# Kernel optimization log

Measured on AMD Instinct MI355X. Metric: run time of the kernel, lower is better.

## Reference

```python
import jax, jax.numpy as jnp
import numpy as np

OFFSETS = (12, 20, 30, 42, 55, 67)  # pixel offsets along shadow direction


def _bilinear_shift(img, dx, dy):
    """Sample img (H,W) at (y+dy, x+dx), bilinear, zero padding.
    Equivalent to F.grid_sample with identity affine_grid + uniform shift
    (align_corners=True): normalized shift d*2/(W-1) == d pixels.
    Separable interpolation (valid because padding is zeros)."""
    H, W = img.shape
    xs = jnp.arange(W, dtype=img.dtype) + dx  # (W,) sample x-coords
    ys = jnp.arange(H, dtype=img.dtype) + dy  # (H,) sample y-coords
    x0f = jnp.floor(xs); wx = xs - x0f
    y0f = jnp.floor(ys); wy = ys - y0f
    x0 = x0f.astype(jnp.int32); x1 = x0 + 1
    y0 = y0f.astype(jnp.int32); y1 = y0 + 1

    def gx(ix):  # gather columns with zero padding
        valid = ((ix >= 0) & (ix < W)).astype(img.dtype)
        return img[:, jnp.clip(ix, 0, W - 1)] * valid[None, :]

    row = gx(x0) * (1.0 - wx)[None, :] + gx(x1) * wx[None, :]  # (H,W)

    def gy(iy):  # gather rows with zero padding
        valid = ((iy >= 0) & (iy < H)).astype(img.dtype)
        return row[jnp.clip(iy, 0, H - 1), :] * valid[:, None]

    return gy(y0) * (1.0 - wy)[:, None] + gy(y1) * wy[:, None]


def _warp_stack(shadow_map, shadow_dir):
    """shadow_map (B,1,H,W), shadow_dir (B,2) -> (B,n_offsets,H,W)."""
    img = shadow_map[:, 0]  # (B,H,W)
    d = jnp.asarray(OFFSETS, dtype=img.dtype)  # (n,)
    dx = shadow_dir[:, 0:1] * d          # (B,n) pixel shift in x
    dy = -shadow_dir[:, 1:2] * d         # (B,n) pixel shift in y
    f = jax.vmap(jax.vmap(_bilinear_shift, in_axes=(None, 0, 0)),
                 in_axes=(0, 0, 0))
    return f(img, dx, dy)  # (B,n,H,W)


def setup_inputs() -> dict:
    key = jax.random.key(0)
    k1, k2, k3, k4, k5 = jax.random.split(key, 5)
    B, C, Hf, Wf = 4, 512, 128, 128
    H, W = 1024, 1024
    n = len(OFFSETS)
    rgb_feat = jax.random.normal(k1, (B, C, Hf, Wf), dtype=jnp.float32)
    shadow_map = jax.random.uniform(k2, (B, 1, H, W), dtype=jnp.float32)
    shadow_dir = jax.random.normal(k3, (B, 2), dtype=jnp.float32)
    shadow_dir = shadow_dir / jnp.linalg.norm(shadow_dir, axis=-1, keepdims=True)
    w_conv = 0.02 * jax.random.normal(k4, (C, n), dtype=jnp.float32)
    b_conv = 0.02 * jax.random.normal(k5, (C,), dtype=jnp.float32)
    gate = jnp.ones((1,), dtype=jnp.float32) * 0.01
    return {"rgb_feat": rgb_feat, "shadow_map": shadow_map,
            "shadow_dir": shadow_dir, "w_conv": w_conv,
            "b_conv": b_conv, "gate": gate}


def reference(rgb_feat, shadow_map, shadow_dir, w_conv, b_conv, gate):
    B, C, Hf, Wf = rgb_feat.shape
    n = len(OFFSETS)
    evidence = _warp_stack(shadow_map, shadow_dir)  # (B,n,H,W)
    # bilinear downsample, align_corners=False, no antialias (matches torch)
    evidence = jax.image.resize(evidence, (B, n, Hf, Wf),
                                method="linear", antialias=False)
    mixed = jnp.einsum("bnhw,cn->bchw", evidence, w_conv) \
            + b_conv[None, :, None, None]
    return rgb_feat + gate[0] * mixed
```

## Files before the change

kernel.cpp:

```cpp
#include <hip/hip_runtime.h>

#define HRES 1024
#define WRES 1024
#define HF   128
#define WF   128
#define NOFF 6
#define CCH  512
#define BB   4
#define CHUNK 16

typedef float vfloat4 __attribute__((ext_vector_type(4)));
typedef vfloat4 uvfloat4 __attribute__((aligned(4)));

__global__ void evidence_kernel(const float* __restrict__ smap,
                                const float* __restrict__ sdir,
                                float* __restrict__ E) {
    int B = blockIdx.x;
    int r   = B & 7;
    int q   = B >> 3;
    int b64 = q >> 3;
    int sub = q & 7;
    int off = 4 * r + sub + (sub >= 4 ? 28 : 0);
    int c   = b64 * 64 + off;
    int t   = c * 256 + threadIdx.x;

    int j = t & (WF - 1);
    int i = (t >> 7) & (HF - 1);
    int k = (t >> 14) % NOFF;
    int b = t / (NOFF << 14);

    const float offs[NOFF] = {12.f, 20.f, 30.f, 42.f, 55.f, 67.f};
    float dirx = sdir[b * 2 + 0];
    float diry = sdir[b * 2 + 1];
    float d  = offs[k];
    float dx = dirx * d;
    float dy = -diry * d;
    float fxf = floorf(dx), fyf = floorf(dy);
    float wx = dx - fxf,    wy = dy - fyf;

    int X0 = 8 * j + 3 + (int)fxf;
    int Y0 = 8 * i + 3 + (int)fyf;

    float wx0 = 0.5f * (1.f - wx), wx1 = 0.5f, wx2 = 0.5f * wx;
    float wyv[3] = {0.5f * (1.f - wy), 0.5f, 0.5f * wy};

    const float* img = smap + (size_t)b * HRES * WRES;
    bool fastx = (X0 >= 0) & (X0 + 3 < WRES);
    float acc = 0.f;
#pragma unroll
    for (int rr = 0; rr < 3; ++rr) {
        int y = Y0 + rr;
        if ((unsigned)y < HRES) {
            const float* rowp = img + (size_t)y * WRES;
            float s0, s1, s2;
            if (fastx) {
                vfloat4 v = *reinterpret_cast<const uvfloat4*>(rowp + X0);
                s0 = v.x; s1 = v.y; s2 = v.z;
            } else {
                s0 = ((unsigned)(X0 + 0) < WRES) ? rowp[X0 + 0] : 0.f;
                s1 = ((unsigned)(X0 + 1) < WRES) ? rowp[X0 + 1] : 0.f;
                s2 = ((unsigned)(X0 + 2) < WRES) ? rowp[X0 + 2] : 0.f;
            }
            acc += (s0 * wx0 + s1 * wx1 + s2 * wx2) * wyv[rr];
        }
    }
    E[t] = acc;
}

__global__ __launch_bounds__(256) void mix_kernel(
        const float* __restrict__ rgb,
        const float* __restrict__ E,
        const float* __restrict__ w_conv,
        const float* __restrict__ b_conv,
        const float* __restrict__ gate,
        float* __restrict__ out) {
    int tile = blockIdx.x;
    int b    = tile >> 4;
    int p    = (tile & 15) * 1024 + threadIdx.x * 4;
    int c0   = blockIdx.y * CHUNK;
    float g  = gate[0];

    vfloat4 e[NOFF];
#pragma unroll
    for (int k = 0; k < NOFF; ++k) {
        e[k] = *reinterpret_cast<const vfloat4*>(
            E + (((size_t)(b * NOFF + k)) << 14) + p);
        e[k] *= g;
    }

    const vfloat4* rgbp = reinterpret_cast<const vfloat4*>(
        rgb + (((size_t)(b * CCH + c0)) << 14) + p);
    vfloat4* outp = reinterpret_cast<vfloat4*>(
        out + (((size_t)(b * CCH + c0)) << 14) + p);
    const int stride4 = (1 << 14) / 4;

#pragma unroll
    for (int c8 = 0; c8 < CHUNK / 8; ++c8) {
        vfloat4 rv[8];
#pragma unroll
        for (int u = 0; u < 8; ++u)
            rv[u] = rgbp[(size_t)(c8 * 8 + u) * stride4];
#pragma unroll
        for (int u = 0; u < 8; ++u) {
            int c  = c8 * 8 + u;
            int cg = c0 + c;
            const float* wrow = w_conv + (size_t)cg * NOFF;
            float w0 = wrow[0], w1 = wrow[1], w2 = wrow[2];
            float w3 = wrow[3], w4 = wrow[4], w5 = wrow[5];
            float bb = g * b_conv[cg];
            vfloat4 o;
            o.x = rv[u].x + bb + e[0].x * w0 + e[1].x * w1 + e[2].x * w2
                               + e[3].x * w3 + e[4].x * w4 + e[5].x * w5;
            o.y = rv[u].y + bb + e[0].y * w0 + e[1].y * w1 + e[2].y * w2
                               + e[3].y * w3 + e[4].y * w4 + e[5].y * w5;
            o.z = rv[u].z + bb + e[0].z * w0 + e[1].z * w1 + e[2].z * w2
                               + e[3].z * w3 + e[4].z * w4 + e[5].z * w5;
            o.w = rv[u].w + bb + e[0].w * w0 + e[1].w * w1 + e[2].w * w2
                               + e[3].w * w3 + e[4].w * w4 + e[5].w * w5;
            __builtin_nontemporal_store(o, outp + (size_t)c * stride4);
        }
    }
}

extern "C" void kernel_launch(void* const* d_in, const int* in_sizes, int n_in,
                              void* d_out, int out_size, void* d_ws, size_t ws_size,
                              hipStream_t stream) {
    const float* rgb    = (const float*)d_in[0];
    const float* smap   = (const float*)d_in[1];
    const float* sdir   = (const float*)d_in[2];
    const float* w_conv = (const float*)d_in[3];
    const float* b_conv = (const float*)d_in[4];
    const float* gate   = (const float*)d_in[5];
    float* out = (float*)d_out;

    float* E = (float*)d_ws;
    evidence_kernel<<<1536, 256, 0, stream>>>(smap, sdir, E);

    dim3 grid_mix(BB * 16, CCH / CHUNK);
    mix_kernel<<<grid_mix, 256, 0, stream>>>(rgb, E, w_conv, b_conv, gate, out);
}
```

Baseline: 50.16 us.

## Fuse evidence computation into mix kernel, recomputing per channel chunk

Removes the separate evidence kernel and its workspace round-trip by computing the six shifted-and-downsampled evidence values directly inside the mix kernel, four adjacent output pixels per thread. This saves a kernel launch and the intermediate write and read. In exchange, every channel-chunk block recomputes the same evidence, multiplying gather loads from the shadow map by the number of chunks.

```diff
diff --git a/kernel.cpp b/kernel.cpp
--- a/kernel.cpp
+++ b/kernel.cpp
@@ -12,64 +12,10 @@
 typedef float vfloat4 __attribute__((ext_vector_type(4)));
 typedef vfloat4 uvfloat4 __attribute__((aligned(4)));
 
-__global__ void evidence_kernel(const float* __restrict__ smap,
-                                const float* __restrict__ sdir,
-                                float* __restrict__ E) {
-    int B = blockIdx.x;
-    int r   = B & 7;
-    int q   = B >> 3;
-    int b64 = q >> 3;
-    int sub = q & 7;
-    int off = 4 * r + sub + (sub >= 4 ? 28 : 0);
-    int c   = b64 * 64 + off;
-    int t   = c * 256 + threadIdx.x;
-
-    int j = t & (WF - 1);
-    int i = (t >> 7) & (HF - 1);
-    int k = (t >> 14) % NOFF;
-    int b = t / (NOFF << 14);
-
-    const float offs[NOFF] = {12.f, 20.f, 30.f, 42.f, 55.f, 67.f};
-    float dirx = sdir[b * 2 + 0];
-    float diry = sdir[b * 2 + 1];
-    float d  = offs[k];
-    float dx = dirx * d;
-    float dy = -diry * d;
-    float fxf = floorf(dx), fyf = floorf(dy);
-    float wx = dx - fxf,    wy = dy - fyf;
-
-    int X0 = 8 * j + 3 + (int)fxf;
-    int Y0 = 8 * i + 3 + (int)fyf;
-
-    float wx0 = 0.5f * (1.f - wx), wx1 = 0.5f, wx2 = 0.5f * wx;
-    float wyv[3] = {0.5f * (1.f - wy), 0.5f, 0.5f * wy};
-
-    const float* img = smap + (size_t)b * HRES * WRES;
-    bool fastx = (X0 >= 0) & (X0 + 3 < WRES);
-    float acc = 0.f;
-#pragma unroll
-    for (int rr = 0; rr < 3; ++rr) {
-        int y = Y0 + rr;
-        if ((unsigned)y < HRES) {
-            const float* rowp = img + (size_t)y * WRES;
-            float s0, s1, s2;
-            if (fastx) {
-                vfloat4 v = *reinterpret_cast<const uvfloat4*>(rowp + X0);
-                s0 = v.x; s1 = v.y; s2 = v.z;
-            } else {
-                s0 = ((unsigned)(X0 + 0) < WRES) ? rowp[X0 + 0] : 0.f;
-                s1 = ((unsigned)(X0 + 1) < WRES) ? rowp[X0 + 1] : 0.f;
-                s2 = ((unsigned)(X0 + 2) < WRES) ? rowp[X0 + 2] : 0.f;
-            }
-            acc += (s0 * wx0 + s1 * wx1 + s2 * wx2) * wyv[rr];
-        }
-    }
-    E[t] = acc;
-}
-
-__global__ __launch_bounds__(256) void mix_kernel(
+__global__ __launch_bounds__(256) void fused_kernel(
         const float* __restrict__ rgb,
-        const float* __restrict__ E,
+        const float* __restrict__ smap,
+        const float* __restrict__ sdir,
         const float* __restrict__ w_conv,
         const float* __restrict__ b_conv,
         const float* __restrict__ gate,
@@ -80,12 +26,57 @@
     int c0   = blockIdx.y * CHUNK;
     float g  = gate[0];
 
+    int i  = p >> 7;
+    int j0 = p & (WF - 1);
+
+    const float* img = smap + (size_t)b * HRES * WRES;
+    float dirx = sdir[b * 2 + 0];
+    float diry = sdir[b * 2 + 1];
+
+    const float offs[NOFF] = {12.f, 20.f, 30.f, 42.f, 55.f, 67.f};
     vfloat4 e[NOFF];
+
 #pragma unroll
     for (int k = 0; k < NOFF; ++k) {
-        e[k] = *reinterpret_cast<const vfloat4*>(
-            E + (((size_t)(b * NOFF + k)) << 14) + p);
-        e[k] *= g;
+        float d  = offs[k];
+        float dx = dirx * d;
+        float dy = -diry * d;
+        float fxf = floorf(dx), fyf = floorf(dy);
+        float wx = dx - fxf,    wy = dy - fyf;
+        int ifx = (int)fxf, ify = (int)fyf;
+
+        int X0 = 8 * j0 + 3 + ifx;
+        int Y0 = 8 * i  + 3 + ify;
+
+        float wx0 = 0.5f * (1.f - wx), wx1 = 0.5f, wx2 = 0.5f * wx;
+        float wyv[3] = {0.5f * (1.f - wy), 0.5f, 0.5f * wy};
+
+        float acc[4] = {0.f, 0.f, 0.f, 0.f};
+#pragma unroll
+        for (int rr = 0; rr < 3; ++rr) {
+            int y = Y0 + rr;
+            if ((unsigned)y < HRES) {
+                const float* rowp = img + (size_t)y * WRES;
+                float wyr = wyv[rr];
+#pragma unroll
+                for (int u = 0; u < 4; ++u) {
+                    int X = X0 + 8 * u;
+                    float s0, s1, s2;
+                    if ((X >= 0) & (X + 3 < WRES)) {
+                        vfloat4 v = *reinterpret_cast<const uvfloat4*>(rowp + X);
+                        s0 = v.x; s1 = v.y; s2 = v.z;
+                    } else {
+                        s0 = ((unsigned)(X + 0) < WRES) ? rowp[X + 0] : 0.f;
+                        s1 = ((unsigned)(X + 1) < WRES) ? rowp[X + 1] : 0.f;
+                        s2 = ((unsigned)(X + 2) < WRES) ? rowp[X + 2] : 0.f;
+                    }
+                    acc[u] += (s0 * wx0 + s1 * wx1 + s2 * wx2) * wyr;
+                }
+            }
+        }
+        vfloat4 ev;
+        ev.x = acc[0]; ev.y = acc[1]; ev.z = acc[2]; ev.w = acc[3];
+        e[k] = ev * g;
     }
 
     const vfloat4* rgbp = reinterpret_cast<const vfloat4*>(
@@ -133,9 +124,7 @@
     const float* gate   = (const float*)d_in[5];
     float* out = (float*)d_out;
 
-    float* E = (float*)d_ws;
-    evidence_kernel<<<1536, 256, 0, stream>>>(smap, sdir, E);
-
-    dim3 grid_mix(BB * 16, CCH / CHUNK);
-    mix_kernel<<<grid_mix, 256, 0, stream>>>(rgb, E, w_conv, b_conv, gate, out);
+    dim3 grid(BB * 16, CCH / CHUNK);
+    fused_kernel<<<grid, 256, 0, stream>>>(rgb, smap, sdir,
+                                           w_conv, b_conv, gate, out);
 }
```

Result: slower. 136.2 us (+171.5%).
